# Kernel tuning notes

Measured on AMD Instinct MI355X. Metric: run time of the kernel, lower is better.

## Reference

```python
import jax, jax.numpy as jnp
import numpy as np

EMBED_DIM = 1024
NUM_HEADS = 16
HEAD_DIM = EMBED_DIM // NUM_HEADS
ROPE_BASE = 10000.0


def setup_inputs() -> dict:
    key = jax.random.key(0)
    ks = jax.random.split(key, 5)
    B, S, E = 4, 2048, EMBED_DIM
    hidden = jax.random.normal(ks[0], (B, S, E), dtype=jnp.float32)
    sc_in = 1.0 / np.sqrt(E)
    qkv_w = jax.random.normal(ks[1], (3 * E, E), dtype=jnp.float32) * sc_in
    qkv_b = jnp.zeros((3 * E,), dtype=jnp.float32)
    proj_w = jax.random.normal(ks[2], (E, E), dtype=jnp.float32) * sc_in
    proj_b = jnp.zeros((E,), dtype=jnp.float32)
    return {"hidden": hidden, "qkv_w": qkv_w, "qkv_b": qkv_b,
            "proj_w": proj_w, "proj_b": proj_b}


def _rope_cos_sin(position_ids, head_dim, base):
    # position_ids: [B, S] int; returns cos/sin of shape [B, 1, S, head_dim]
    inv_freq = 1.0 / (base ** (jnp.arange(0, head_dim, 2, dtype=jnp.float32) / head_dim))
    freqs = position_ids.astype(jnp.float32)[..., None] * inv_freq  # [B,S,hd/2]
    emb = jnp.concatenate([freqs, freqs], axis=-1)                  # [B,S,hd]
    return jnp.cos(emb)[:, None], jnp.sin(emb)[:, None]


def _rotate_half(x):
    x1, x2 = jnp.split(x, 2, axis=-1)
    return jnp.concatenate([-x2, x1], axis=-1)


def reference(hidden, qkv_w, qkv_b, proj_w, proj_b):
    B, S, E = hidden.shape
    H, hd = NUM_HEADS, HEAD_DIM
    qkv = hidden @ qkv_w.T + qkv_b                    # [B,S,3E]
    qkv = qkv.reshape(B, S, 3, H, hd).transpose(2, 0, 3, 1, 4)  # [3,B,H,S,hd]
    q, k, v = qkv[0], qkv[1], qkv[2]
    pos = jnp.broadcast_to(jnp.arange(S)[None, :], (B, S))
    cos, sin = _rope_cos_sin(pos, hd, ROPE_BASE)      # [B,1,S,hd]
    q = q * cos + _rotate_half(q) * sin
    k = k * cos + _rotate_half(k) * sin
    scale = 1.0 / jnp.sqrt(jnp.float32(hd))
    scores = jnp.einsum("bhsd,bhtd->bhst", q, k) * scale
    attn = jax.nn.softmax(scores, axis=-1)
    out = jnp.einsum("bhst,bhtd->bhsd", attn, v)      # [B,H,S,hd]
    out = out.transpose(0, 2, 1, 3).reshape(B, S, E)
    return out @ proj_w.T + proj_b
```

## Files before the change

### kernel.cpp

```cpp
#include <hip/hip_runtime.h>
#include <cstdint>
#include <cstddef>

typedef _Float16 f16;
typedef __attribute__((ext_vector_type(4))) float f32x4;
typedef __attribute__((ext_vector_type(8))) _Float16 f16x8;
typedef __attribute__((ext_vector_type(4))) _Float16 f16x4;

#define S_SEQ 2048
#define E_DIM 1024

#define OFF_HID   0ull
#define OFF_QKVW  8388608ull
#define OFF_PROJW 11534336ull
#define OFF_Q     12582912ull
#define OFF_K     20971520ull
#define OFF_VT    29360128ull
#define OFF_AO    37748736ull

__device__ __forceinline__ void async_copy16(const void* g, void* l) {
  __builtin_amdgcn_global_load_lds(
      (const __attribute__((address_space(1))) unsigned int*)g,
      (__attribute__((address_space(3))) unsigned int*)l, 16, 0, 0);
}

__device__ __forceinline__ float fast_exp2(float x) {
#if __has_builtin(__builtin_amdgcn_exp2f)
  return __builtin_amdgcn_exp2f(x);
#else
  return __expf(x * 0.6931471805599453f);
#endif
}

__global__ __launch_bounds__(256) void cvt_kernel(const float* __restrict__ hid,
                                                  const float* __restrict__ qw,
                                                  const float* __restrict__ pw,
                                                  f16* __restrict__ ws) {
  long i = (long)blockIdx.x * 256 + threadIdx.x;
  const float* src;
  f16* dst;
  long idx;
  if (i < 2097152L) { src = hid; dst = ws + OFF_HID;  idx = i; }
  else if (i < 2883584L) { src = qw; dst = ws + OFF_QKVW; idx = i - 2097152L; }
  else { src = pw; dst = ws + OFF_PROJW; idx = i - 2883584L; }
  float4 v = *(const float4*)(src + idx * 4);
  f16x4 o = { (f16)v.x, (f16)v.y, (f16)v.z, (f16)v.w };
  *(f16x4*)(dst + idx * 4) = o;
}

template <int MODE>
__global__ __launch_bounds__(256)
void gemm_kernel(const f16* __restrict__ A, const f16* __restrict__ Bm,
                 const float* __restrict__ bias,
                 f16* __restrict__ q_out, f16* __restrict__ k_out,
                 f16* __restrict__ vT_out, float* __restrict__ f_out) {
  __shared__ __align__(16) f16 As[128 * 64];
  __shared__ __align__(16) f16 Bs[128 * 64];
  const int tid = threadIdx.x;
  const int wave = tid >> 6;
  const int lane = tid & 63;
  const int q4 = lane >> 4;
  const int l16 = lane & 15;
  const int m0 = blockIdx.y * 128;
  const int n0 = blockIdx.x * 128;
  const int wr = (wave >> 1) * 64;
  const int wc = (wave & 1) * 64;
  f32x4 acc[4][4] = {};

  const int srow = tid >> 3;
  const int scol = (tid & 7) * 8;

  for (int k0 = 0; k0 < 1024; k0 += 64) {
    __syncthreads();
    for (int p = 0; p < 4; ++p) {
      int row = p * 32 + srow;
      async_copy16(A + (size_t)(m0 + row) * 1024 + k0 + scol,
                   As + (size_t)(p * 2048) + (size_t)wave * 512);
      async_copy16(Bm + (size_t)(n0 + row) * 1024 + k0 + scol,
                   Bs + (size_t)(p * 2048) + (size_t)wave * 512);
    }
    __syncthreads();
    for (int kf = 0; kf < 2; ++kf) {
      f16x8 af[4], bf[4];
      for (int mt = 0; mt < 4; ++mt)
        af[mt] = *(const f16x8*)&As[(wr + mt * 16 + l16) * 64 + kf * 32 + q4 * 8];
      for (int nt = 0; nt < 4; ++nt)
        bf[nt] = *(const f16x8*)&Bs[(wc + nt * 16 + l16) * 64 + kf * 32 + q4 * 8];
      for (int mt = 0; mt < 4; ++mt)
        for (int nt = 0; nt < 4; ++nt)
          acc[mt][nt] = __builtin_amdgcn_mfma_f32_16x16x32_f16(af[mt], bf[nt],
                                                               acc[mt][nt], 0, 0, 0);
    }
  }

  if constexpr (MODE == 0) {
    const int bx = blockIdx.x;
    const int part = bx >> 3;
    const int h = (((bx & 7) * 128) + wc) >> 6;
    float bv[4];
    for (int nt = 0; nt < 4; ++nt) bv[nt] = bias[n0 + wc + nt * 16 + l16];
    if (part < 2) {
      f16* outp = (part == 0) ? q_out : k_out;
      const float qscale = (part == 0) ? 0.18033688011112042f : 1.0f;
      float invf[2];
      for (int nt = 0; nt < 2; ++nt)
        invf[nt] = __expf(-(float)(nt * 16 + l16) * 0.2878231366242557f);
      for (int mt = 0; mt < 4; ++mt) {
        int mbase = m0 + wr + mt * 16 + q4 * 4;
        for (int r = 0; r < 4; ++r) {
          int mm = mbase + r;
          int b = mm >> 11, s = mm & 2047;
          size_t rowb = ((size_t)((b * 16 + h) * 2048 + s)) * 64;
          for (int nt = 0; nt < 2; ++nt) {
            float x1 = acc[mt][nt][r] + bv[nt];
            float x2 = acc[mt][nt + 2][r] + bv[nt + 2];
            float ang = (float)s * invf[nt];
            float sn, cs;
            __sincosf(ang, &sn, &cs);
            float o1 = (x1 * cs - x2 * sn) * qscale;
            float o2 = (x2 * cs + x1 * sn) * qscale;
            int d1 = nt * 16 + l16;
            outp[rowb + d1] = (f16)o1;
            outp[rowb + d1 + 32] = (f16)o2;
          }
        }
      }
    } else {
      for (int mt = 0; mt < 4; ++mt) {
        int mbase = m0 + wr + mt * 16 + q4 * 4;
        int b = mbase >> 11, s0 = mbase & 2047;
        for (int nt = 0; nt < 4; ++nt) {
          int d = nt * 16 + l16;
          size_t basei = ((size_t)((b * 16 + h) * 64 + d)) * 2048 + s0;
          f16x4 pk;
          for (int r = 0; r < 4; ++r) pk[r] = (f16)(acc[mt][nt][r] + bv[nt]);
          *(f16x4*)&vT_out[basei] = pk;
        }
      }
    }
  } else {
    float bv[4];
    for (int nt = 0; nt < 4; ++nt) bv[nt] = bias[n0 + wc + nt * 16 + l16];
    for (int mt = 0; mt < 4; ++mt)
      for (int r = 0; r < 4; ++r) {
        int mm = m0 + wr + mt * 16 + q4 * 4 + r;
        for (int nt = 0; nt < 4; ++nt)
          f_out[(size_t)mm * 1024 + n0 + wc + nt * 16 + l16] = acc[mt][nt][r] + bv[nt];
      }
  }
}

__global__ __launch_bounds__(256, 4)
void attn_kernel(const f16* __restrict__ Qg, const f16* __restrict__ Kg,
                 const f16* __restrict__ VTg, f16* __restrict__ AOg) {
  __shared__ __align__(16) f16 smem[2 * 64 * 72];
  f16* Ks = smem;
  f16* Vs = smem + 64 * 72;
  const int tid = threadIdx.x;
  const int wave = tid >> 6, lane = tid & 63;
  const int q4 = lane >> 4, l16 = lane & 15;
  const int qt = blockIdx.x, bh = blockIdx.y;
  const f16* Qb = Qg + (size_t)bh * (S_SEQ * 64);
  const f16* Kb = Kg + (size_t)bh * (S_SEQ * 64);
  const f16* Vb = VTg + (size_t)bh * (64 * S_SEQ);
  const int ws0 = wave * 32;

  f16x8 qf[2][2];
  for (int sn = 0; sn < 2; ++sn)
    for (int kf = 0; kf < 2; ++kf)
      qf[sn][kf] = *(const f16x8*)(Qb + (size_t)(qt * 128 + ws0 + sn * 16 + l16) * 64
                                      + kf * 32 + q4 * 8);

  f32x4 o[4][2] = {};
  float lsum[2] = {0.f, 0.f};

  const int srow = tid >> 3;
  const int scol = (tid & 7) * 8;

  for (int tt = 0; tt < 32; ++tt) {
    const int t0 = tt * 64;
    __syncthreads();
    for (int p = 0; p < 2; ++p) {
      int rr = p * 32 + srow;
      *(int4*)(Ks + rr * 72 + scol) = *(const int4*)(Kb + (size_t)(t0 + rr) * 64 + scol);
      *(int4*)(Vs + rr * 72 + scol) = *(const int4*)(Vb + (size_t)rr * 2048 + t0 + scol);
    }
    __syncthreads();

    f32x4 st[4][2];
    for (int tm = 0; tm < 4; ++tm) {
      f16x8 k0 = *(const f16x8*)(Ks + (tm * 16 + l16) * 72 + q4 * 8);
      f16x8 k1 = *(const f16x8*)(Ks + (tm * 16 + l16) * 72 + 32 + q4 * 8);
      for (int sn = 0; sn < 2; ++sn) {
        f32x4 c = {0.f, 0.f, 0.f, 0.f};
        c = __builtin_amdgcn_mfma_f32_16x16x32_f16(k0, qf[sn][0], c, 0, 0, 0);
        c = __builtin_amdgcn_mfma_f32_16x16x32_f16(k1, qf[sn][1], c, 0, 0, 0);
        st[tm][sn] = c;
      }
    }

    for (int sn = 0; sn < 2; ++sn) {
      float rs = 0.f;
      for (int tm = 0; tm < 4; ++tm)
        for (int r = 0; r < 4; ++r) {
          float p = fast_exp2(st[tm][sn][r]);
          st[tm][sn][r] = p;
          rs += p;
        }
      lsum[sn] += rs;
    }

    for (int tm = 0; tm < 4; ++tm) {
      f16x4 vfr[4];
      for (int dm = 0; dm < 4; ++dm)
        vfr[dm] = *(const f16x4*)(Vs + (dm * 16 + l16) * 72 + tm * 16 + q4 * 4);
      for (int sn = 0; sn < 2; ++sn) {
        f16x4 pfr;
        pfr[0] = (f16)st[tm][sn][0];
        pfr[1] = (f16)st[tm][sn][1];
        pfr[2] = (f16)st[tm][sn][2];
        pfr[3] = (f16)st[tm][sn][3];
        for (int dm = 0; dm < 4; ++dm)
          o[dm][sn] = __builtin_amdgcn_mfma_f32_16x16x16f16(vfr[dm], pfr,
                                                            o[dm][sn], 0, 0, 0);
      }
    }
  }

  float inv_l[2];
  for (int sn = 0; sn < 2; ++sn) {
    float l = lsum[sn];
    l += __shfl_xor(l, 16, 64);
    l += __shfl_xor(l, 32, 64);
    inv_l[sn] = 1.0f / l;
  }
  __syncthreads();
  f16* Ot = smem;
  for (int sn = 0; sn < 2; ++sn) {
    int so = ws0 + sn * 16 + l16;
    for (int dm = 0; dm < 4; ++dm) {
      f16x4 w;
      w[0] = (f16)(o[dm][sn][0] * inv_l[sn]);
      w[1] = (f16)(o[dm][sn][1] * inv_l[sn]);
      w[2] = (f16)(o[dm][sn][2] * inv_l[sn]);
      w[3] = (f16)(o[dm][sn][3] * inv_l[sn]);
      *(f16x4*)(Ot + so * 72 + dm * 16 + q4 * 4) = w;
    }
  }
  __syncthreads();
  const int b = bh >> 4, h = bh & 15;
  const int sr = tid >> 1, dh = (tid & 1) * 32;
  size_t gbase = ((size_t)(b * 2048 + qt * 128 + sr)) * 1024 + h * 64 + dh;
  for (int c = 0; c < 4; ++c) {
    f16x8 v = *(const f16x8*)(Ot + sr * 72 + dh + c * 8);
    *(f16x8*)(AOg + gbase + c * 8) = v;
  }
}

extern "C" void kernel_launch(void* const* d_in, const int* in_sizes, int n_in,
                              void* d_out, int out_size, void* d_ws, size_t ws_size,
                              hipStream_t stream) {
  const float* hid   = (const float*)d_in[0];
  const float* qkvw  = (const float*)d_in[1];
  const float* qkvb  = (const float*)d_in[2];
  const float* projw = (const float*)d_in[3];
  const float* projb = (const float*)d_in[4];
  float* out = (float*)d_out;
  f16* ws = (f16*)d_ws;

  cvt_kernel<<<12288, 256, 0, stream>>>(hid, qkvw, projw, ws);
  gemm_kernel<0><<<dim3(24, 64), 256, 0, stream>>>(
      ws + OFF_HID, ws + OFF_QKVW, qkvb,
      ws + OFF_Q, ws + OFF_K, ws + OFF_VT, nullptr);
  attn_kernel<<<dim3(16, 64), 256, 0, stream>>>(
      ws + OFF_Q, ws + OFF_K, ws + OFF_VT, ws + OFF_AO);
  gemm_kernel<1><<<dim3(8, 64), 256, 0, stream>>>(
      ws + OFF_AO, ws + OFF_PROJW, projb,
      nullptr, nullptr, nullptr, out);
}
```

Before: 290.1 us.

## Double-buffer GEMM LDS tiles and register-prefetch K/V tiles in attention

The GEMM kernel now uses two LDS buffers with a K-step of 32 and issues the async global-to-LDS copy for the next tile before computing on the current one, which leaves one barrier per iteration. The attention kernel loads the next K/V tile into registers while the current tile is being computed, so global load latency overlaps with the MFMA work. This costs more registers and halves the work per GEMM iteration, which increases loop and barrier overhead relative to compute.

Measured after the change: 350.1 us. 20.7% more time.

```diff
diff --git a/kernel.cpp b/kernel.cpp
--- a/kernel.cpp
+++ b/kernel.cpp
@@ -54,8 +54,8 @@
                  const float* __restrict__ bias,
                  f16* __restrict__ q_out, f16* __restrict__ k_out,
                  f16* __restrict__ vT_out, float* __restrict__ f_out) {
-  __shared__ __align__(16) f16 As[128 * 64];
-  __shared__ __align__(16) f16 Bs[128 * 64];
+  __shared__ __align__(16) f16 As[2][128 * 32];
+  __shared__ __align__(16) f16 Bs[2][128 * 32];
   const int tid = threadIdx.x;
   const int wave = tid >> 6;
   const int lane = tid & 63;
@@ -67,30 +67,35 @@
   const int wc = (wave & 1) * 64;
   f32x4 acc[4][4] = {};
 
-  const int srow = tid >> 3;
-  const int scol = (tid & 7) * 8;
-
-  for (int k0 = 0; k0 < 1024; k0 += 64) {
+  const int srow = tid >> 2;
+  const int scol = (tid & 3) * 8;
+
+  auto stage = [&](int k0, int b) {
+    for (int p = 0; p < 2; ++p) {
+      int row = p * 64 + srow;
+      async_copy16(A + (size_t)(m0 + row) * 1024 + k0 + scol,
+                   &As[b][(size_t)(p * 256 + wave * 64) * 8]);
+      async_copy16(Bm + (size_t)(n0 + row) * 1024 + k0 + scol,
+                   &Bs[b][(size_t)(p * 256 + wave * 64) * 8]);
+    }
+  };
+
+  stage(0, 0);
+  __syncthreads();
+  int buf = 0;
+  for (int k0 = 0; k0 < 1024; k0 += 32) {
+    if (k0 + 32 < 1024) stage(k0 + 32, buf ^ 1);
+    f16x8 af[4], bf[4];
+    for (int mt = 0; mt < 4; ++mt)
+      af[mt] = *(const f16x8*)&As[buf][(wr + mt * 16 + l16) * 32 + q4 * 8];
+    for (int nt = 0; nt < 4; ++nt)
+      bf[nt] = *(const f16x8*)&Bs[buf][(wc + nt * 16 + l16) * 32 + q4 * 8];
+    for (int mt = 0; mt < 4; ++mt)
+      for (int nt = 0; nt < 4; ++nt)
+        acc[mt][nt] = __builtin_amdgcn_mfma_f32_16x16x32_f16(af[mt], bf[nt],
+                                                             acc[mt][nt], 0, 0, 0);
     __syncthreads();
-    for (int p = 0; p < 4; ++p) {
-      int row = p * 32 + srow;
-      async_copy16(A + (size_t)(m0 + row) * 1024 + k0 + scol,
-                   As + (size_t)(p * 2048) + (size_t)wave * 512);
-      async_copy16(Bm + (size_t)(n0 + row) * 1024 + k0 + scol,
-                   Bs + (size_t)(p * 2048) + (size_t)wave * 512);
-    }
-    __syncthreads();
-    for (int kf = 0; kf < 2; ++kf) {
-      f16x8 af[4], bf[4];
-      for (int mt = 0; mt < 4; ++mt)
-        af[mt] = *(const f16x8*)&As[(wr + mt * 16 + l16) * 64 + kf * 32 + q4 * 8];
-      for (int nt = 0; nt < 4; ++nt)
-        bf[nt] = *(const f16x8*)&Bs[(wc + nt * 16 + l16) * 64 + kf * 32 + q4 * 8];
-      for (int mt = 0; mt < 4; ++mt)
-        for (int nt = 0; nt < 4; ++nt)
-          acc[mt][nt] = __builtin_amdgcn_mfma_f32_16x16x32_f16(af[mt], bf[nt],
-                                                               acc[mt][nt], 0, 0, 0);
-    }
+    buf ^= 1;
   }
 
   if constexpr (MODE == 0) {
@@ -177,15 +182,25 @@
   const int srow = tid >> 3;
   const int scol = (tid & 7) * 8;
 
+  int4 kreg[2], vreg[2];
+  auto prefetch = [&](int t0) {
+    for (int p = 0; p < 2; ++p) {
+      int rr = p * 32 + srow;
+      kreg[p] = *(const int4*)(Kb + (size_t)(t0 + rr) * 64 + scol);
+      vreg[p] = *(const int4*)(Vb + (size_t)rr * 2048 + t0 + scol);
+    }
+  };
+  prefetch(0);
+
   for (int tt = 0; tt < 32; ++tt) {
-    const int t0 = tt * 64;
     __syncthreads();
     for (int p = 0; p < 2; ++p) {
       int rr = p * 32 + srow;
-      *(int4*)(Ks + rr * 72 + scol) = *(const int4*)(Kb + (size_t)(t0 + rr) * 64 + scol);
-      *(int4*)(Vs + rr * 72 + scol) = *(const int4*)(Vb + (size_t)rr * 2048 + t0 + scol);
+      *(int4*)(Ks + rr * 72 + scol) = kreg[p];
+      *(int4*)(Vs + rr * 72 + scol) = vreg[p];
     }
     __syncthreads();
+    if (tt + 1 < 32) prefetch((tt + 1) * 64);
 
     f32x4 st[4][2];
     for (int tm = 0; tm < 4; ++tm) {
```
